# Optimization experiments

Measured on AMD Instinct MI355X. Metric: run time of the kernel, lower is better.

Reference implementation:

```python
import jax, jax.numpy as jnp
import numpy as np

# S6Layer dims: d_model=256; internal d_state=max(8,16//2)=8; expand=max(1.5,2*0.75)=1.5 -> d_inner=384
B, L, DM = 8, 4096, 256
DI, DS = 384, 8
CHUNK = 32  # seq_len > 64 path: chunked scan, state resets to 0 at every chunk (faithful to source)
EPS = 1e-5


def setup_inputs() -> dict:
    key = jax.random.key(0)
    ks = jax.random.split(key, 8)
    def w(k, shape, s=0.02):
        return jax.random.normal(k, shape, jnp.float32) * s
    return {
        "x": jax.random.normal(ks[0], (B, L, DM), jnp.float32),
        "gamma": jnp.ones((DM,), jnp.float32),
        "beta": jnp.zeros((DM,), jnp.float32),
        "W_in": w(ks[1], (3 * DI, DM)),
        "b_in": jnp.zeros((3 * DI,), jnp.float32),
        "W_dt": w(ks[2], (DI, DI)),
        "b_dt": jnp.zeros((DI,), jnp.float32),
        "A_log": jax.random.normal(ks[3], (DI, DS), jnp.float32),
        "D_vec": jax.random.normal(ks[4], (DI,), jnp.float32),
        "W_out": w(ks[5], (DM, DI)),
        "b_out": jnp.zeros((DM,), jnp.float32),
    }


def _layernorm(x, g, b):
    mu = jnp.mean(x, axis=-1, keepdims=True)
    var = jnp.mean(jnp.square(x - mu), axis=-1, keepdims=True)
    return (x - mu) * jax.lax.rsqrt(var + EPS) * g + b


def _chunked_scan(xp, dt, A):
    # xp, dt: [B, L, DI]; A: [DI, DS]. Each CHUNK-length block scans from h=0
    # (the torch code never propagates h across chunks for seq_len > 64).
    C = L // CHUNK
    xr = xp.reshape(B, C, CHUNK, DI)
    dtr = dt.reshape(B, C, CHUNK, DI)
    dA = jnp.exp(dtr[..., None] * A)              # [B, C, T, DI, DS]
    dA_t = jnp.moveaxis(dA, 2, 0)                 # [T, B, C, DI, DS]
    x_t = jnp.moveaxis(xr, 2, 0)                  # [T, B, C, DI]

    def step(h, inp):
        dA_i, x_i = inp
        h = h * dA_i + x_i[..., None]             # broadcast x over DS
        return h, jnp.sum(h, axis=-1)             # y_i: [B, C, DI]

    h0 = jnp.zeros((B, C, DI, DS), xp.dtype)
    _, ys = jax.lax.scan(step, h0, (dA_t, x_t))   # ys: [T, B, C, DI]
    return jnp.moveaxis(ys, 0, 2).reshape(B, L, DI)


def reference(x, gamma, beta, W_in, b_in, W_dt, b_dt, A_log, D_vec, W_out, b_out):
    residual = x
    xn = _layernorm(x, gamma, beta)
    xz = xn @ W_in.T + b_in                       # [B, L, 3*DI]
    x_proj, z, dt_in = jnp.split(xz, 3, axis=-1)
    x_proj = jax.nn.silu(x_proj)
    z = jax.nn.silu(z)
    dt = jax.nn.softplus(dt_in @ W_dt.T + b_dt)   # [B, L, DI]
    A = -jnp.exp(A_log)                           # [DI, DS]
    y = _chunked_scan(x_proj, dt, A)
    y = y * z + x_proj * D_vec
    return y @ W_out.T + b_out + residual
```

## Files before the change

### kernel.cpp

```cpp
#include <hip/hip_runtime.h>
#include <stdint.h>

#define B_  8
#define L_  4096
#define DM  256
#define DI  384
#define DS  8
#define M_  (B_*L_)

typedef float f32x4 __attribute__((ext_vector_type(4)));
typedef short s16x8 __attribute__((ext_vector_type(8)));

#define AS1(p) ((__attribute__((address_space(1))) void*)(p))
#define AS3(p) ((__attribute__((address_space(3))) void*)(p))

__device__ __forceinline__ unsigned short f2bf(float f) {
  union { float f; uint32_t u; } v; v.f = f;
  uint32_t r = v.u + 0x7FFFu + ((v.u >> 16) & 1u);
  return (unsigned short)(r >> 16);
}
__device__ __forceinline__ float bf2f(unsigned short h) {
  union { uint32_t u; float f; } v; v.u = ((uint32_t)h) << 16;
  return v.f;
}
__device__ __forceinline__ float silu_f(float x) {
  return x * __builtin_amdgcn_rcpf(1.f + __expf(-x));
}

__global__ __launch_bounds__(256) void cvt_kernel(
    const float* __restrict__ w0, const float* __restrict__ w2,
    const float* __restrict__ b_in,
    unsigned short* __restrict__ o0, unsigned short* __restrict__ o2,
    float* __restrict__ biasc) {
  int i = blockIdx.x * 256 + threadIdx.x;
  if (i < 3*DI*DM) o0[i] = f2bf(w0[i]);
  if (i < DM*DI)   o2[i] = f2bf(w2[i]);
  if (i < 2*DI)    biasc[i] = b_in[i];
}

__global__ __launch_bounds__(256) void prep_kernel(
    const float* __restrict__ W_in, const float* __restrict__ b_in,
    const float* __restrict__ W_dt, const float* __restrict__ b_dt,
    unsigned short* __restrict__ winb, float* __restrict__ biasc) {
  int nb = blockIdx.x;
  if (nb < DI) {
    int c = threadIdx.x;
    float acc = 0.f;
    for (int k = 0; k < DI; ++k)
      acc += W_dt[(size_t)nb*DI + k] * W_in[(size_t)(2*DI + k)*DM + c];
    winb[(size_t)(2*DI + nb)*DM + c] = f2bf(acc);
  } else {
    int n = (nb - DI)*256 + threadIdx.x;
    if (n < DI) {
      float acc = b_dt[n];
      for (int k = 0; k < DI; ++k)
        acc += W_dt[(size_t)n*DI + k] * b_in[2*DI + k];
      biasc[2*DI + n] = acc;
    }
  }
}

__global__ __launch_bounds__(256) void ln_kernel(
    const float* __restrict__ x, const float* __restrict__ gamma, const float* __restrict__ beta,
    unsigned short* __restrict__ xn) {
  int token = blockIdx.x * 4 + (threadIdx.x >> 6);
  int lane  = threadIdx.x & 63;
  const float4 v = *(const float4*)(x + (size_t)token*DM + lane*4);
  float s  = v.x + v.y + v.z + v.w;
  float ss = v.x*v.x + v.y*v.y + v.z*v.z + v.w*v.w;
  #pragma unroll
  for (int off = 32; off > 0; off >>= 1) {
    s  += __shfl_xor(s,  off, 64);
    ss += __shfl_xor(ss, off, 64);
  }
  float mean = s * (1.f/DM);
  float var  = ss * (1.f/DM) - mean*mean;
  float rstd = rsqrtf(var + 1e-5f);
  const float4 g = *(const float4*)(gamma + lane*4);
  const float4 b = *(const float4*)(beta  + lane*4);
  ushort4 o;
  o.x = f2bf((v.x - mean)*rstd*g.x + b.x);
  o.y = f2bf((v.y - mean)*rstd*g.y + b.y);
  o.z = f2bf((v.z - mean)*rstd*g.z + b.z);
  o.w = f2bf((v.w - mean)*rstd*g.w + b.w);
  *(ushort4*)(xn + (size_t)token*DM + lane*4) = o;
}

template<int EPI, int KSTEPS, int MT>
__global__ __launch_bounds__(256, 3) void gemm_ws(
    const unsigned short* __restrict__ A,
    const unsigned short* __restrict__ Bw,
    const float* __restrict__ bias,
    unsigned short* __restrict__ o_xp, unsigned short* __restrict__ o_z,
    unsigned short* __restrict__ o_dt,
    const float* __restrict__ resid, float* __restrict__ o_f)
{
  constexpr int K    = KSTEPS * 32;
  constexpr int CPR  = K / 8;
  __shared__ unsigned short sB[64*K];
  __shared__ unsigned short sC[(EPI == 3) ? 2 : 4*32*72];

  const int t    = threadIdx.x;
  const int lane = t & 63;
  const int w    = t >> 6;
  const int fr   = lane & 15;
  const int fq   = lane >> 4;
  const int wm   = w * 32;

  const int q    = blockIdx.y * 128 + blockIdx.x;
  const int bx2  = (q & 7) * 16 + ((q >> 3) & 15);
  const int by2  = q >> 7;
  const int mbase0 = bx2 * (128 * MT);
  const int nbase  = by2 * 64;

  #pragma unroll
  for (int i = 0; i < (64*CPR)/256; ++i) {
    int c   = i*256 + t;
    int row = c / CPR;
    int j   = c - row*CPR;
    int jp  = (j & ~7) | ((j & 7) ^ (row & 7));
    __builtin_amdgcn_global_load_lds(AS1(Bw + (size_t)(nbase + row)*K + jp*8),
                                     AS3(sB + c*8), 16, 0, 0);
  }

  const unsigned short* sBrE = sB + (size_t)fr*K + ( fq      ^ (fr & 7))*8;
  const unsigned short* sBrO = sB + (size_t)fr*K + ((fq | 4) ^ (fr & 7))*8;

  float bvv[4];
  #pragma unroll
  for (int ni = 0; ni < 4; ++ni) bvv[ni] = bias[nbase + ni*16 + fr];

  unsigned short* sCw = sC + w*(32*72);

  __syncthreads();

  #pragma unroll
  for (int mt = 0; mt < MT; ++mt) {
    const int mbase = mbase0 + mt*128;
    const unsigned short* gA0 = A + (size_t)(mbase + wm + fr)*K + fq*8;
    const unsigned short* gA1 = gA0 + (size_t)16*K;

    f32x4 acc[2][4];
    #pragma unroll
    for (int mi = 0; mi < 2; ++mi)
      #pragma unroll
      for (int ni = 0; ni < 4; ++ni) acc[mi][ni] = (f32x4){0.f, 0.f, 0.f, 0.f};

    #pragma unroll
    for (int kt = 0; kt < KSTEPS; ++kt) {
      s16x8 a0 = *(const s16x8*)(gA0 + kt*32);
      s16x8 a1 = *(const s16x8*)(gA1 + kt*32);
      const unsigned short* bb = (kt & 1) ? sBrO : sBrE;
      s16x8 bfr[4];
      #pragma unroll
      for (int ni = 0; ni < 4; ++ni)
        bfr[ni] = *(const s16x8*)(bb + ni*16*K + (kt >> 1)*64);
      #pragma unroll
      for (int ni = 0; ni < 4; ++ni) {
        acc[0][ni] = __builtin_amdgcn_mfma_f32_16x16x32_bf16(a0, bfr[ni], acc[0][ni], 0, 0, 0);
        acc[1][ni] = __builtin_amdgcn_mfma_f32_16x16x32_bf16(a1, bfr[ni], acc[1][ni], 0, 0, 0);
      }
    }

    if constexpr (EPI == 3) {
      #pragma unroll
      for (int ni = 0; ni < 4; ++ni) {
        int gn = nbase + ni*16 + fr;
        #pragma unroll
        for (int mi = 0; mi < 2; ++mi) {
          int gm0 = mbase + wm + mi*16 + fq*4;
          #pragma unroll
          for (int r = 0; r < 4; ++r) {
            size_t gm = (size_t)(gm0 + r);
            o_f[gm*DM + gn] = acc[mi][ni][r] + bvv[ni] + resid[gm*DM + gn];
          }
        }
      }
    } else {
      const bool do_silu = (by2 < 12);
      #pragma unroll
      for (int ni = 0; ni < 4; ++ni) {
        int cn = ni*16 + fr;
        #pragma unroll
        for (int mi = 0; mi < 2; ++mi) {
          int rm0 = mi*16 + fq*4;
          #pragma unroll
          for (int r = 0; r < 4; ++r) {
            float c = acc[mi][ni][r] + bvv[ni];
            c = do_silu ? silu_f(c)
                        : ((c > 20.f) ? c : __logf(1.f + __expf(c)));
            sCw[(rm0 + r)*72 + cn] = f2bf(c);
          }
        }
      }
      asm volatile("s_waitcnt lgkmcnt(0)" ::: "memory");
      unsigned short* dst = (by2 < 6) ? o_xp : (by2 < 12) ? o_z : o_dt;
      int colbase = (by2 % 6) * 64;
      const int rr = lane >> 3, cc = (lane & 7) * 8;
      #pragma unroll
      for (int it = 0; it < 4; ++it) {
        int row32 = rr + it*8;
        s16x8 v = *(const s16x8*)(sCw + row32*72 + cc);
        *(s16x8*)(dst + (size_t)(mbase + wm + row32)*DI + colbase + cc) = v;
      }
    }
  }
}

__global__ __launch_bounds__(384) void scan_kernel(
    const unsigned short* __restrict__ xp, unsigned short* dt_yz,
    const unsigned short* __restrict__ zb, const float* __restrict__ A_log,
    const float* __restrict__ D_vec) {
  int g  = blockIdx.x;
  int di = threadIdx.x;
  size_t base = (size_t)g * 32 * DI + di;
  float a[DS];
  #pragma unroll
  for (int s = 0; s < DS; ++s) a[s] = -__expf(A_log[di*DS + s]);
  float Dv = D_vec[di];
  float h[DS] = {0.f,0.f,0.f,0.f,0.f,0.f,0.f,0.f};
  for (int tt = 0; tt < 32; ++tt) {
    size_t idx = base + (size_t)tt * DI;
    float xv  = bf2f(xp[idx]);
    float dtv = bf2f(dt_yz[idx]);
    float y = 0.f;
    #pragma unroll
    for (int s = 0; s < DS; ++s) {
      h[s] = h[s] * __expf(dtv * a[s]) + xv;
      y += h[s];
    }
    float zv = bf2f(zb[idx]);
    dt_yz[idx] = f2bf(y * zv + xv * Dv);
  }
}

extern "C" void kernel_launch(void* const* d_in, const int* in_sizes, int n_in,
                              void* d_out, int out_size, void* d_ws, size_t ws_size,
                              hipStream_t stream) {
  const float* x     = (const float*)d_in[0];
  const float* gamma = (const float*)d_in[1];
  const float* beta  = (const float*)d_in[2];
  const float* W_in  = (const float*)d_in[3];
  const float* b_in  = (const float*)d_in[4];
  const float* W_dt  = (const float*)d_in[5];
  const float* b_dt  = (const float*)d_in[6];
  const float* A_log = (const float*)d_in[7];
  const float* D_vec = (const float*)d_in[8];
  const float* W_out = (const float*)d_in[9];
  const float* b_out = (const float*)d_in[10];
  float* out = (float*)d_out;

  char* ws = (char*)d_ws;
  size_t off = 0;
  auto alloc = [&](size_t bytes) -> char* {
    char* p = ws + off; off += (bytes + 255) & ~(size_t)255; return p;
  };
  unsigned short* xn    = (unsigned short*)alloc((size_t)M_*DM*2);
  unsigned short* xpb   = (unsigned short*)alloc((size_t)M_*DI*2);
  unsigned short* zb    = (unsigned short*)alloc((size_t)M_*DI*2);
  unsigned short* dtb   = (unsigned short*)alloc((size_t)M_*DI*2);
  unsigned short* winb  = (unsigned short*)alloc((size_t)3*DI*DM*2);
  unsigned short* woutb = (unsigned short*)alloc((size_t)DM*DI*2);
  float*          biasc = (float*)alloc((size_t)3*DI*4);

  cvt_kernel<<<dim3((3*DI*DM + 255)/256), 256, 0, stream>>>(W_in, W_out, b_in, winb, woutb, biasc);
  prep_kernel<<<dim3(DI + 2), 256, 0, stream>>>(W_in, b_in, W_dt, b_dt, winb, biasc);
  ln_kernel<<<dim3(M_/4), 256, 0, stream>>>(x, gamma, beta, xn);
  gemm_ws<1, 8, 2><<<dim3(128, (3*DI)/64), 256, 0, stream>>>(
      xn, winb, biasc, xpb, zb, dtb, nullptr, nullptr);
  scan_kernel<<<dim3(M_/32), DI, 0, stream>>>(xpb, dtb, zb, A_log, D_vec);
  gemm_ws<3, 12, 2><<<dim3(128, DM/64), 256, 0, stream>>>(
      dtb, woutb, b_out, nullptr, nullptr, nullptr, x, out);
}
```

Measured before the change: 217.4 us.

## Fuse input GEMM epilogue with chunked scan in one kernel via LDS

Replaces the separate input-projection GEMM and scan kernel with one kernel. Each block computes the x, z and dt tiles for 128 tokens and 64 channels, keeps them in swizzled LDS, then runs the 32-step chunk scan directly from LDS. This removes the write and re-read of three bf16 intermediate tensors and one launch. In exchange it needs larger LDS per block (occupancy bound drops to 2), reloads the weight panel three times per block, and each block reads its xn tile three times.

```diff
diff --git a/kernel.cpp b/kernel.cpp
--- a/kernel.cpp
+++ b/kernel.cpp
@@ -86,19 +86,125 @@
   *(ushort4*)(xn + (size_t)token*DM + lane*4) = o;
 }
 
-template<int EPI, int KSTEPS, int MT>
-__global__ __launch_bounds__(256, 3) void gemm_ws(
+__global__ __launch_bounds__(256, 2) void s6_head(
+    const unsigned short* __restrict__ xn,
+    const unsigned short* __restrict__ Wb,
+    const float* __restrict__ biasc,
+    const float* __restrict__ A_log, const float* __restrict__ D_vec,
+    unsigned short* __restrict__ yz)
+{
+  constexpr int K = 256, CPR = K/8;
+  __shared__ unsigned short sB[64*K];
+  __shared__ unsigned short sOut[3][128*64];
+  const int t    = threadIdx.x;
+  const int lane = t & 63;
+  const int w    = t >> 6;
+  const int fr   = lane & 15;
+  const int fq   = lane >> 4;
+  const int wm   = w * 32;
+
+  const int q      = blockIdx.x;
+  const int u      = q >> 3;
+  const int mtile  = (q & 7) * 32 + (u & 31);
+  const int panel  = u >> 5;
+  const int mbase  = mtile * 128;
+  const int chbase = panel * 64;
+
+  const unsigned short* gA0 = xn + (size_t)(mbase + wm + fr)*K + fq*8;
+  const unsigned short* gA1 = gA0 + (size_t)16*K;
+  const unsigned short* sBrE = sB + (size_t)fr*K + ( fq      ^ (fr & 7))*8;
+  const unsigned short* sBrO = sB + (size_t)fr*K + ((fq | 4) ^ (fr & 7))*8;
+
+  #pragma unroll
+  for (int sub = 0; sub < 3; ++sub) {
+    const int nb = sub*DI + chbase;
+    #pragma unroll
+    for (int i = 0; i < (64*CPR)/256; ++i) {
+      int c   = i*256 + t;
+      int row = c / CPR;
+      int j   = c - row*CPR;
+      int jp  = (j & ~7) | ((j & 7) ^ (row & 7));
+      __builtin_amdgcn_global_load_lds(AS1(Wb + (size_t)(nb + row)*K + jp*8),
+                                       AS3(sB + c*8), 16, 0, 0);
+    }
+    __syncthreads();
+
+    f32x4 acc[2][4];
+    #pragma unroll
+    for (int mi = 0; mi < 2; ++mi)
+      #pragma unroll
+      for (int ni = 0; ni < 4; ++ni) acc[mi][ni] = (f32x4){0.f, 0.f, 0.f, 0.f};
+
+    #pragma unroll
+    for (int kt = 0; kt < 8; ++kt) {
+      s16x8 a0 = *(const s16x8*)(gA0 + kt*32);
+      s16x8 a1 = *(const s16x8*)(gA1 + kt*32);
+      const unsigned short* bb = (kt & 1) ? sBrO : sBrE;
+      s16x8 bfr[4];
+      #pragma unroll
+      for (int ni = 0; ni < 4; ++ni)
+        bfr[ni] = *(const s16x8*)(bb + ni*16*K + (kt >> 1)*64);
+      #pragma unroll
+      for (int ni = 0; ni < 4; ++ni) {
+        acc[0][ni] = __builtin_amdgcn_mfma_f32_16x16x32_bf16(a0, bfr[ni], acc[0][ni], 0, 0, 0);
+        acc[1][ni] = __builtin_amdgcn_mfma_f32_16x16x32_bf16(a1, bfr[ni], acc[1][ni], 0, 0, 0);
+      }
+    }
+
+    #pragma unroll
+    for (int ni = 0; ni < 4; ++ni) {
+      float bv = biasc[nb + ni*16 + fr];
+      int cn = (ni*16 + fr) ^ (fq << 4);
+      #pragma unroll
+      for (int mi = 0; mi < 2; ++mi) {
+        int rm0 = wm + mi*16 + fq*4;
+        #pragma unroll
+        for (int r = 0; r < 4; ++r) {
+          float c = acc[mi][ni][r] + bv;
+          c = (sub < 2) ? silu_f(c)
+                        : ((c > 20.f) ? c : __logf(1.f + __expf(c)));
+          sOut[sub][(rm0 + r)*64 + cn] = f2bf(c);
+        }
+      }
+    }
+    __syncthreads();
+  }
+
+  {
+    const int c  = t >> 6;
+    const int d  = t & 63;
+    const int ch = chbase + d;
+    float a[DS], h[DS];
+    #pragma unroll
+    for (int s = 0; s < DS; ++s) { a[s] = -__expf(A_log[ch*DS + s]); h[s] = 0.f; }
+    float Dv = D_vec[ch];
+    unsigned short* yzp = yz + (size_t)(mbase + c*32)*DI + ch;
+    for (int tt = 0; tt < 32; ++tt) {
+      int idx = (c*32 + tt)*64 + (d ^ (((tt >> 2) & 3) << 4));
+      float xv  = bf2f(sOut[0][idx]);
+      float zv  = bf2f(sOut[1][idx]);
+      float dtv = bf2f(sOut[2][idx]);
+      float y = 0.f;
+      #pragma unroll
+      for (int s = 0; s < DS; ++s) {
+        h[s] = h[s] * __expf(dtv * a[s]) + xv;
+        y += h[s];
+      }
+      yzp[(size_t)tt*DI] = f2bf(y * zv + xv * Dv);
+    }
+  }
+}
+
+template<int KSTEPS, int MT>
+__global__ __launch_bounds__(256, 3) void gemm_out(
     const unsigned short* __restrict__ A,
     const unsigned short* __restrict__ Bw,
     const float* __restrict__ bias,
-    unsigned short* __restrict__ o_xp, unsigned short* __restrict__ o_z,
-    unsigned short* __restrict__ o_dt,
     const float* __restrict__ resid, float* __restrict__ o_f)
 {
   constexpr int K    = KSTEPS * 32;
   constexpr int CPR  = K / 8;
   __shared__ unsigned short sB[64*K];
-  __shared__ unsigned short sC[(EPI == 3) ? 2 : 4*32*72];
 
   const int t    = threadIdx.x;
   const int lane = t & 63;
@@ -130,8 +236,6 @@
   #pragma unroll
   for (int ni = 0; ni < 4; ++ni) bvv[ni] = bias[nbase + ni*16 + fr];
 
-  unsigned short* sCw = sC + w*(32*72);
-
   __syncthreads();
 
   #pragma unroll
@@ -162,75 +266,19 @@
       }
     }
 
-    if constexpr (EPI == 3) {
-      #pragma unroll
-      for (int ni = 0; ni < 4; ++ni) {
-        int gn = nbase + ni*16 + fr;
+    #pragma unroll
+    for (int ni = 0; ni < 4; ++ni) {
+      int gn = nbase + ni*16 + fr;
+      #pragma unroll
+      for (int mi = 0; mi < 2; ++mi) {
+        int gm0 = mbase + wm + mi*16 + fq*4;
         #pragma unroll
-        for (int mi = 0; mi < 2; ++mi) {
-          int gm0 = mbase + wm + mi*16 + fq*4;
-          #pragma unroll
-          for (int r = 0; r < 4; ++r) {
-            size_t gm = (size_t)(gm0 + r);
-            o_f[gm*DM + gn] = acc[mi][ni][r] + bvv[ni] + resid[gm*DM + gn];
-          }
+        for (int r = 0; r < 4; ++r) {
+          size_t gm = (size_t)(gm0 + r);
+          o_f[gm*DM + gn] = acc[mi][ni][r] + bvv[ni] + resid[gm*DM + gn];
         }
       }
-    } else {
-      const bool do_silu = (by2 < 12);
-      #pragma unroll
-      for (int ni = 0; ni < 4; ++ni) {
-        int cn = ni*16 + fr;
-        #pragma unroll
-        for (int mi = 0; mi < 2; ++mi) {
-          int rm0 = mi*16 + fq*4;
-          #pragma unroll
-          for (int r = 0; r < 4; ++r) {
-            float c = acc[mi][ni][r] + bvv[ni];
-            c = do_silu ? silu_f(c)
-                        : ((c > 20.f) ? c : __logf(1.f + __expf(c)));
-            sCw[(rm0 + r)*72 + cn] = f2bf(c);
-          }
-        }
-      }
-      asm volatile("s_waitcnt lgkmcnt(0)" ::: "memory");
-      unsigned short* dst = (by2 < 6) ? o_xp : (by2 < 12) ? o_z : o_dt;
-      int colbase = (by2 % 6) * 64;
-      const int rr = lane >> 3, cc = (lane & 7) * 8;
-      #pragma unroll
-      for (int it = 0; it < 4; ++it) {
-        int row32 = rr + it*8;
-        s16x8 v = *(const s16x8*)(sCw + row32*72 + cc);
-        *(s16x8*)(dst + (size_t)(mbase + wm + row32)*DI + colbase + cc) = v;
-      }
-    }
-  }
-}
-
-__global__ __launch_bounds__(384) void scan_kernel(
-    const unsigned short* __restrict__ xp, unsigned short* dt_yz,
-    const unsigned short* __restrict__ zb, const float* __restrict__ A_log,
-    const float* __restrict__ D_vec) {
-  int g  = blockIdx.x;
-  int di = threadIdx.x;
-  size_t base = (size_t)g * 32 * DI + di;
-  float a[DS];
-  #pragma unroll
-  for (int s = 0; s < DS; ++s) a[s] = -__expf(A_log[di*DS + s]);
-  float Dv = D_vec[di];
-  float h[DS] = {0.f,0.f,0.f,0.f,0.f,0.f,0.f,0.f};
-  for (int tt = 0; tt < 32; ++tt) {
-    size_t idx = base + (size_t)tt * DI;
-    float xv  = bf2f(xp[idx]);
-    float dtv = bf2f(dt_yz[idx]);
-    float y = 0.f;
-    #pragma unroll
-    for (int s = 0; s < DS; ++s) {
-      h[s] = h[s] * __expf(dtv * a[s]) + xv;
-      y += h[s];
-    }
-    float zv = bf2f(zb[idx]);
-    dt_yz[idx] = f2bf(y * zv + xv * Dv);
+    }
   }
 }
 
@@ -256,9 +304,7 @@
     char* p = ws + off; off += (bytes + 255) & ~(size_t)255; return p;
   };
   unsigned short* xn    = (unsigned short*)alloc((size_t)M_*DM*2);
-  unsigned short* xpb   = (unsigned short*)alloc((size_t)M_*DI*2);
-  unsigned short* zb    = (unsigned short*)alloc((size_t)M_*DI*2);
-  unsigned short* dtb   = (unsigned short*)alloc((size_t)M_*DI*2);
+  unsigned short* yzb   = (unsigned short*)alloc((size_t)M_*DI*2);
   unsigned short* winb  = (unsigned short*)alloc((size_t)3*DI*DM*2);
   unsigned short* woutb = (unsigned short*)alloc((size_t)DM*DI*2);
   float*          biasc = (float*)alloc((size_t)3*DI*4);
@@ -266,9 +312,7 @@
   cvt_kernel<<<dim3((3*DI*DM + 255)/256), 256, 0, stream>>>(W_in, W_out, b_in, winb, woutb, biasc);
   prep_kernel<<<dim3(DI + 2), 256, 0, stream>>>(W_in, b_in, W_dt, b_dt, winb, biasc);
   ln_kernel<<<dim3(M_/4), 256, 0, stream>>>(x, gamma, beta, xn);
-  gemm_ws<1, 8, 2><<<dim3(128, (3*DI)/64), 256, 0, stream>>>(
-      xn, winb, biasc, xpb, zb, dtb, nullptr, nullptr);
-  scan_kernel<<<dim3(M_/32), DI, 0, stream>>>(xpb, dtb, zb, A_log, D_vec);
-  gemm_ws<3, 12, 2><<<dim3(128, DM/64), 256, 0, stream>>>(
-      dtb, woutb, b_out, nullptr, nullptr, nullptr, x, out);
-}
+  s6_head<<<dim3(6 * 256), 256, 0, stream>>>(xn, winb, biasc, A_log, D_vec, yzb);
+  gemm_out<12, 2><<<dim3(128, DM/64), 256, 0, stream>>>(
+      yzb, woutb, b_out, x, out);
+}
```

Result: no change. 218.7 us (+0.6%).
